# Kernel optimization log

Hardware: AMD Instinct MI355X
Metric: run time of the kernel (lower is better)

## Reference

```python
import jax, jax.numpy as jnp
import numpy as np

B, MAXN = 256, 192
N_ATOMS = 64 + (np.arange(B) % 129)          # ragged sizes 64..192, sum = 32641
TOTAL = int(N_ATOMS.sum())
EPS = 1e-18                                   # torch cosine_similarity eps
DIV_EPS = 1e-3                                # D + 0.001 in the original


def _safe_sqrt(sq):
    # sqrt with zero gradient at 0 (matches torch.norm subgradient at 0)
    pos = sq > 0
    return jnp.where(pos, jnp.sqrt(jnp.where(pos, sq, 1.0)), 0.0)


def setup_inputs() -> dict:
    key = jax.random.key(0)
    k1, k2 = jax.random.split(key)
    partial_forces = jax.random.normal(k1, (TOTAL, MAXN, 3), dtype=jnp.float32)
    positions = 2.0 * jax.random.normal(k2, (TOTAL, 3), dtype=jnp.float32)
    n_atoms = jnp.asarray(N_ATOMS, dtype=jnp.int32)
    return {"partial_forces": partial_forces, "positions": positions, "n_atoms": n_atoms}


def _loss(partial_forces, positions):
    n = N_ATOMS  # static ragged sizes
    row_mol = np.repeat(np.arange(B), n)
    row_idx = np.concatenate([np.arange(k) for k in n])
    # scatter ragged rows into padded [B, MAXN, ...]
    P = jnp.zeros((B, MAXN, MAXN, 3), partial_forces.dtype).at[row_mol, row_idx].set(partial_forces)
    pos = jnp.zeros((B, MAXN, 3), positions.dtype).at[row_mol, row_idx].set(positions)

    valid = np.arange(MAXN)[None, :] < n[:, None]            # [B,N]
    pair = valid[:, :, None] & valid[:, None, :]             # [B,N,N] (includes diagonal)
    offdiag = pair & ~np.eye(MAXN, dtype=bool)[None]         # diag-zeroing mask
    n_f = jnp.asarray(n, jnp.float32)

    r = pos[:, :, None, :] - pos[:, None, :, :]              # [B,N,N,3]
    D = _safe_sqrt(jnp.sum(r * r, -1))                       # [B,N,N]
    Pn = _safe_sqrt(jnp.sum(P * P, -1))                      # [B,N,N]
    Pt = jax.lax.stop_gradient(jnp.swapaxes(P, 1, 2))        # partials.T.clone().detach()
    Ptn = jax.lax.stop_gradient(jnp.swapaxes(Pn, 1, 2))

    # term 1: cos(P_ij, P_ji.detach) / (D+1e-3) summed over i, mean over j, then * mean(diag mask) = *(n-1)/n
    cos_pp = jnp.sum(P * Pt, -1) / jnp.maximum(Pn * Ptn, EPS)
    s1 = jnp.where(pair, cos_pp / (D + DIV_EPS), 0.0).sum(1).sum(-1) / n_f
    term1 = s1 * (n_f - 1.0) / n_f

    # term 2: (||P_ij|| - ||P_ji||.detach)^2 summed over i, mean over j
    term2 = jnp.where(pair, (Pn - Ptn) ** 2, 0.0).sum(1).sum(-1) / n_f

    # term 3: -|mask * cos(P_ij, r_ij)| / (D+1e-3) summed over i, mean over j
    cos_pr = jnp.sum(P * r, -1) / jnp.maximum(Pn * D, EPS)
    masked = jnp.where(offdiag, cos_pr, 0.0)
    term3 = (-jnp.abs(masked) / (D + DIV_EPS)).sum(1).sum(-1) / n_f

    return jnp.mean(term1 + term2 + term3)


def reference(partial_forces, positions, n_atoms):
    return _loss(partial_forces, positions)
```

## Files before the change

### kernel.cpp

```cpp
#include <hip/hip_runtime.h>

#define BMOL 256
#define PPM 300
#define NSLOT (BMOL * 8)

__device__ __forceinline__ int mol_n(int b) { return 64 + (b % 129); }
__device__ __forceinline__ int mol_off(int b) {
  int full = b / 129, rem = b % 129;
  return full * 16512 + 64 * rem + (rem * (rem - 1)) / 2;
}
__device__ __forceinline__ float frcp(float x) { return __builtin_amdgcn_rcpf(x); }

__global__ __launch_bounds__(256) void zero_acc(float* acc) {
  const int idx = blockIdx.x * 256 + threadIdx.x;
  if (idx < NSLOT) acc[idx * 16] = 0.0f;
}

__global__ __launch_bounds__(256) void pair_oct(const float* __restrict__ pf,
                                                const float* __restrict__ pos,
                                                float* __restrict__ acc) {
  const int wave = threadIdx.x >> 6;
  const int lane = threadIdx.x & 63;
  const int u = blockIdx.x * 4 + wave;
  const int b = u / PPM;
  const int pr = u - b * PPM;
  int oj = (int)((__builtin_amdgcn_sqrtf(8.f * (float)pr + 1.f) - 1.f) * 0.5f);
  if ((oj + 1) * (oj + 2) / 2 <= pr) ++oj;
  if (oj * (oj + 1) / 2 > pr) --oj;
  const int oi = pr - oj * (oj + 1) / 2;
  const int n = mol_n(b);
  const int j0 = oj * 8, i0 = oi * 8;
  if (j0 >= n) return;
  const int off = mol_off(b);

  const int ki = lane >> 3, kj = lane & 7;
  const int i = i0 + ki, j = j0 + kj;
  const bool act = (i < n) && (j < n);
  const int ic = min(i, n - 1), jc = min(j, n - 1);

  const float* ap = pf + (size_t)(off + ic) * 576 + 3 * jc;
  const float ax = ap[0], ay = ap[1], az = ap[2];
  const float* cp = pf + (size_t)(off + jc) * 576 + 3 * ic;
  const float cx = cp[0], cy = cp[1], cz = cp[2];
  const float* pip = pos + (size_t)(off + ic) * 3;
  const float pix = pip[0], piy = pip[1], piz = pip[2];
  const float* pjp = pos + (size_t)(off + jc) * 3;
  const float pjx = pjp[0], pjy = pjp[1], pjz = pjp[2];
  __builtin_amdgcn_sched_barrier(0);

  const float nf  = (float)n;
  const float sc1 = (nf - 1.f) / (nf * nf);
  const float sc2 = 1.f / nf;
  const bool  dbl = (oi < oj);

  const float rx = pix - pjx, ry = piy - pjy, rz = piz - pjz;
  const float d2 = rx * rx + ry * ry + rz * rz;
  const float D  = (d2 > 0.f) ? __builtin_amdgcn_sqrtf(d2) : 0.f;
  const float pn2 = ax * ax + ay * ay + az * az;
  const float Pn  = (pn2 > 0.f) ? __builtin_amdgcn_sqrtf(pn2) : 0.f;
  const float qn2 = cx * cx + cy * cy + cz * cz;
  const float Qn  = (qn2 > 0.f) ? __builtin_amdgcn_sqrtf(qn2) : 0.f;
  const float invDeps = frcp(D + 1e-3f);
  const float pq = Pn * Qn;

  const float dot_pp = ax * cx + ay * cy + az * cz;
  const float t1 = dot_pp * frcp(fmaxf(pq, 1e-18f)) * invDeps;
  const float dpn = Pn - Qn;
  const float t2 = dpn * dpn;
  const float dot_ar = ax * rx + ay * ry + az * rz;
  const float dot_cr = cx * rx + cy * ry + cz * rz;
  const float t3a = fabsf(dot_ar) * frcp(fmaxf(Pn * D, 1e-18f)) * invDeps;
  const float t3c = fabsf(dot_cr) * frcp(fmaxf(Qn * D, 1e-18f)) * invDeps;

  float val;
  if (dbl) {
    val = sc1 * 2.f * t1 + sc2 * (2.f * t2 - (t3a + t3c));
  } else {
    val = sc1 * t1 + sc2 * (t2 - ((j != i) ? t3a : 0.f));
  }
  float accv = act ? val : 0.f;

  for (int o = 32; o > 0; o >>= 1) accv += __shfl_xor(accv, o, 64);
  if (lane == 0) atomicAdd(&acc[(b * 8 + (u & 7)) * 16], accv);
}

__global__ __launch_bounds__(256) void finalize(const float* __restrict__ acc,
                                                float* __restrict__ out) {
  __shared__ float red[4];
  float v = 0.f;
  for (int s = threadIdx.x; s < NSLOT; s += 256) v += acc[s * 16];
  for (int o = 32; o > 0; o >>= 1) v += __shfl_xor(v, o, 64);
  if ((threadIdx.x & 63) == 0) red[threadIdx.x >> 6] = v;
  __syncthreads();
  if (threadIdx.x == 0)
    out[0] = (red[0] + red[1] + red[2] + red[3]) * (1.0f / (float)BMOL);
}

extern "C" void kernel_launch(void* const* d_in, const int* in_sizes, int n_in,
                              void* d_out, int out_size, void* d_ws, size_t ws_size,
                              hipStream_t stream) {
  const float* pf  = (const float*)d_in[0];
  const float* pos = (const float*)d_in[1];
  float* acc = (float*)d_ws;
  float* out = (float*)d_out;

  hipLaunchKernelGGL(zero_acc, dim3(NSLOT / 256), dim3(256), 0, stream, acc);
  hipLaunchKernelGGL(pair_oct, dim3(BMOL * PPM / 4), dim3(256), 0, stream, pf, pos, acc);
  hipLaunchKernelGGL(finalize, dim3(1), dim3(256), 0, stream, acc, out);
}
```

Before: 29.89 us.

## Use 16x16 pair tiles per wave and replace atomics with per-wave partials

Each wave now covers a 16x16 block of the upper-triangular pair tiles (four 8x8 sub-tiles, three on the diagonal) instead of one 8x8 tile, which cuts the number of waves and reuses the position loads. Per-wave sums are written directly to a partials array, so the zeroing kernel and the atomics go away, and finalize reduces the array. Blocks are remapped in a strided pattern across the grid and launch bounds request 4 blocks per SIMD. More loads are in flight per lane and register pressure rises.

```diff
diff --git a/kernel.cpp b/kernel.cpp
--- a/kernel.cpp
+++ b/kernel.cpp
@@ -1,8 +1,8 @@
 #include <hip/hip_runtime.h>
 
 #define BMOL 256
-#define PPM 300
-#define NSLOT (BMOL * 8)
+#define PPM16 78
+#define NW (BMOL * PPM16)
 
 __device__ __forceinline__ int mol_n(int b) { return 64 + (b % 129); }
 __device__ __forceinline__ int mol_off(int b) {
@@ -11,84 +11,111 @@
 }
 __device__ __forceinline__ float frcp(float x) { return __builtin_amdgcn_rcpf(x); }
 
-__global__ __launch_bounds__(256) void zero_acc(float* acc) {
-  const int idx = blockIdx.x * 256 + threadIdx.x;
-  if (idx < NSLOT) acc[idx * 16] = 0.0f;
-}
-
-__global__ __launch_bounds__(256) void pair_oct(const float* __restrict__ pf,
-                                                const float* __restrict__ pos,
-                                                float* __restrict__ acc) {
+__global__ __launch_bounds__(256, 4) void pair16(const float* __restrict__ pf,
+                                                 const float* __restrict__ pos,
+                                                 float* __restrict__ part) {
   const int wave = threadIdx.x >> 6;
   const int lane = threadIdx.x & 63;
-  const int u = blockIdx.x * 4 + wave;
-  const int b = u / PPM;
-  const int pr = u - b * PPM;
+  const int bid = (blockIdx.x & 7) * (gridDim.x >> 3) + (blockIdx.x >> 3);
+  const int u = bid * 4 + wave;
+  const int b = u / PPM16;
+  const int pr = u - b * PPM16;
   int oj = (int)((__builtin_amdgcn_sqrtf(8.f * (float)pr + 1.f) - 1.f) * 0.5f);
   if ((oj + 1) * (oj + 2) / 2 <= pr) ++oj;
   if (oj * (oj + 1) / 2 > pr) --oj;
   const int oi = pr - oj * (oj + 1) / 2;
   const int n = mol_n(b);
-  const int j0 = oj * 8, i0 = oi * 8;
-  if (j0 >= n) return;
+  const int j0 = oj * 16, i0 = oi * 16;
+  if (j0 >= n) {
+    if (lane == 0) part[u] = 0.f;
+    return;
+  }
   const int off = mol_off(b);
+  const int ki = lane >> 3, kj = lane & 7;
+  const bool diag = (oi == oj);
 
-  const int ki = lane >> 3, kj = lane & 7;
-  const int i = i0 + ki, j = j0 + kj;
-  const bool act = (i < n) && (j < n);
-  const int ic = min(i, n - 1), jc = min(j, n - 1);
-
-  const float* ap = pf + (size_t)(off + ic) * 576 + 3 * jc;
-  const float ax = ap[0], ay = ap[1], az = ap[2];
-  const float* cp = pf + (size_t)(off + jc) * 576 + 3 * ic;
-  const float cx = cp[0], cy = cp[1], cz = cp[2];
-  const float* pip = pos + (size_t)(off + ic) * 3;
-  const float pix = pip[0], piy = pip[1], piz = pip[2];
-  const float* pjp = pos + (size_t)(off + jc) * 3;
-  const float pjx = pjp[0], pjy = pjp[1], pjz = pjp[2];
+  float Pi[2][3], Pj[2][3], A[2][2][3], C[2][2][3];
+  bool act[2][2];
+#pragma unroll
+  for (int di = 0; di < 2; ++di) {
+    const int icl = min(i0 + 8 * di + ki, n - 1);
+    const float* pp = pos + (size_t)(off + icl) * 3;
+    Pi[di][0] = pp[0]; Pi[di][1] = pp[1]; Pi[di][2] = pp[2];
+  }
+#pragma unroll
+  for (int dj = 0; dj < 2; ++dj) {
+    const int jcl = min(j0 + 8 * dj + kj, n - 1);
+    const float* pp = pos + (size_t)(off + jcl) * 3;
+    Pj[dj][0] = pp[0]; Pj[dj][1] = pp[1]; Pj[dj][2] = pp[2];
+  }
+#pragma unroll
+  for (int di = 0; di < 2; ++di)
+#pragma unroll
+    for (int dj = 0; dj < 2; ++dj) {
+      if (diag && di == 1 && dj == 0) continue;
+      const int i = i0 + 8 * di + ki, j = j0 + 8 * dj + kj;
+      act[di][dj] = (i < n) && (j < n);
+      const int icl = min(i, n - 1), jcl = min(j, n - 1);
+      const float* ap = pf + (size_t)(off + icl) * 576 + 3 * jcl;
+      A[di][dj][0] = ap[0]; A[di][dj][1] = ap[1]; A[di][dj][2] = ap[2];
+      const float* cp = pf + (size_t)(off + jcl) * 576 + 3 * icl;
+      C[di][dj][0] = cp[0]; C[di][dj][1] = cp[1]; C[di][dj][2] = cp[2];
+    }
   __builtin_amdgcn_sched_barrier(0);
 
   const float nf  = (float)n;
   const float sc1 = (nf - 1.f) / (nf * nf);
   const float sc2 = 1.f / nf;
-  const bool  dbl = (oi < oj);
+  float accv = 0.f;
 
-  const float rx = pix - pjx, ry = piy - pjy, rz = piz - pjz;
-  const float d2 = rx * rx + ry * ry + rz * rz;
-  const float D  = (d2 > 0.f) ? __builtin_amdgcn_sqrtf(d2) : 0.f;
-  const float pn2 = ax * ax + ay * ay + az * az;
-  const float Pn  = (pn2 > 0.f) ? __builtin_amdgcn_sqrtf(pn2) : 0.f;
-  const float qn2 = cx * cx + cy * cy + cz * cz;
-  const float Qn  = (qn2 > 0.f) ? __builtin_amdgcn_sqrtf(qn2) : 0.f;
-  const float invDeps = frcp(D + 1e-3f);
-  const float pq = Pn * Qn;
+#pragma unroll
+  for (int di = 0; di < 2; ++di)
+#pragma unroll
+    for (int dj = 0; dj < 2; ++dj) {
+      if (diag && di == 1 && dj == 0) continue;
+      const bool dbl = !diag || (di == 0 && dj == 1);
+      const int i = i0 + 8 * di + ki, j = j0 + 8 * dj + kj;
+      const float ax = A[di][dj][0], ay = A[di][dj][1], az = A[di][dj][2];
+      const float cx = C[di][dj][0], cy = C[di][dj][1], cz = C[di][dj][2];
+      const float rx = Pi[di][0] - Pj[dj][0];
+      const float ry = Pi[di][1] - Pj[dj][1];
+      const float rz = Pi[di][2] - Pj[dj][2];
+      const float d2 = rx * rx + ry * ry + rz * rz;
+      const float D  = (d2 > 0.f) ? __builtin_amdgcn_sqrtf(d2) : 0.f;
+      const float pn2 = ax * ax + ay * ay + az * az;
+      const float Pn  = (pn2 > 0.f) ? __builtin_amdgcn_sqrtf(pn2) : 0.f;
+      const float qn2 = cx * cx + cy * cy + cz * cz;
+      const float Qn  = (qn2 > 0.f) ? __builtin_amdgcn_sqrtf(qn2) : 0.f;
+      const float invDeps = frcp(D + 1e-3f);
+      const float pq = Pn * Qn;
 
-  const float dot_pp = ax * cx + ay * cy + az * cz;
-  const float t1 = dot_pp * frcp(fmaxf(pq, 1e-18f)) * invDeps;
-  const float dpn = Pn - Qn;
-  const float t2 = dpn * dpn;
-  const float dot_ar = ax * rx + ay * ry + az * rz;
-  const float dot_cr = cx * rx + cy * ry + cz * rz;
-  const float t3a = fabsf(dot_ar) * frcp(fmaxf(Pn * D, 1e-18f)) * invDeps;
-  const float t3c = fabsf(dot_cr) * frcp(fmaxf(Qn * D, 1e-18f)) * invDeps;
+      const float dot_pp = ax * cx + ay * cy + az * cz;
+      const float t1 = dot_pp * frcp(fmaxf(pq, 1e-18f)) * invDeps;
+      const float dpn = Pn - Qn;
+      const float t2 = dpn * dpn;
+      const float dot_ar = ax * rx + ay * ry + az * rz;
+      const float dot_cr = cx * rx + cy * ry + cz * rz;
+      const float t3a = fabsf(dot_ar) * frcp(fmaxf(Pn * D, 1e-18f)) * invDeps;
+      const float t3c = fabsf(dot_cr) * frcp(fmaxf(Qn * D, 1e-18f)) * invDeps;
 
-  float val;
-  if (dbl) {
-    val = sc1 * 2.f * t1 + sc2 * (2.f * t2 - (t3a + t3c));
-  } else {
-    val = sc1 * t1 + sc2 * (t2 - ((j != i) ? t3a : 0.f));
-  }
-  float accv = act ? val : 0.f;
+      float val;
+      if (dbl) {
+        val = sc1 * 2.f * t1 + sc2 * (2.f * t2 - (t3a + t3c));
+      } else {
+        val = sc1 * t1 + sc2 * (t2 - ((j != i) ? t3a : 0.f));
+      }
+      accv += act[di][dj] ? val : 0.f;
+    }
 
   for (int o = 32; o > 0; o >>= 1) accv += __shfl_xor(accv, o, 64);
-  if (lane == 0) atomicAdd(&acc[(b * 8 + (u & 7)) * 16], accv);
+  if (lane == 0) part[u] = accv;
 }
 
-__global__ __launch_bounds__(256) void finalize(const float* __restrict__ acc,
+__global__ __launch_bounds__(256) void finalize(const float* __restrict__ part,
                                                 float* __restrict__ out) {
   __shared__ float red[4];
   float v = 0.f;
-  for (int s = threadIdx.x; s < NSLOT; s += 256) v += acc[s * 16];
+  for (int s = threadIdx.x; s < NW; s += 256) v += part[s];
   for (int o = 32; o > 0; o >>= 1) v += __shfl_xor(v, o, 64);
   if ((threadIdx.x & 63) == 0) red[threadIdx.x >> 6] = v;
   __syncthreads();
@@ -99,12 +126,11 @@
 extern "C" void kernel_launch(void* const* d_in, const int* in_sizes, int n_in,
                               void* d_out, int out_size, void* d_ws, size_t ws_size,
                               hipStream_t stream) {
-  const float* pf  = (const float*)d_in[0];
-  const float* pos = (const float*)d_in[1];
-  float* acc = (float*)d_ws;
-  float* out = (float*)d_out;
+  const float* pf   = (const float*)d_in[0];
+  const float* pos  = (const float*)d_in[1];
+  float* part = (float*)d_ws;
+  float* out  = (float*)d_out;
 
-  hipLaunchKernelGGL(zero_acc, dim3(NSLOT / 256), dim3(256), 0, stream, acc);
-  hipLaunchKernelGGL(pair_oct, dim3(BMOL * PPM / 4), dim3(256), 0, stream, pf, pos, acc);
-  hipLaunchKernelGGL(finalize, dim3(1), dim3(256), 0, stream, acc, out);
+  hipLaunchKernelGGL(pair16, dim3(NW / 4), dim3(256), 0, stream, pf, pos, part);
+  hipLaunchKernelGGL(finalize, dim3(1), dim3(256), 0, stream, part, out);
 }
```

Measured after the change: 37.43 us. +25.2%, slower.
